# Performance work log

Measured on AMD Instinct MI355X. Metric: run time of the kernel, lower is better.

## Reference

```python
import jax, jax.numpy as jnp
import numpy as np

N, M, K = 4096, 256, 32
W_EPS = 1e-6


def _spd(key, n, k):
    # well-conditioned SPD precision matrices: A A^T / k + I
    a = jax.random.normal(key, (n, k, k), dtype=jnp.float32)
    return jnp.matmul(a, jnp.swapaxes(a, -1, -2)) / k + jnp.eye(k, dtype=jnp.float32)


def setup_inputs() -> dict:
    key = jax.random.key(0)
    k1, k2, k3, k4 = jax.random.split(key, 4)
    W = jax.random.uniform(k1, (N, M), dtype=jnp.float32)
    mu_s = jax.random.normal(k2, (N, K), dtype=jnp.float32)
    omega_child = _spd(k3, N, K)
    omega_parent = _spd(k4, M, K)
    return {"W": W, "mu_s": mu_s, "omega_child": omega_child, "omega_parent": omega_parent}


def reference(W, mu_s, omega_child, omega_parent):
    # mask out negligible memberships (original skips w < 1e-6)
    wT = W.T                                   # (M, N)
    mask = wT >= W_EPS
    w = jnp.where(mask, wT, 0.0)

    # v_i = inv(omega_child_i) @ mu_s_i  -> batched solve, (N, K)
    v = jnp.linalg.solve(omega_child, mu_s[..., None])[..., 0]

    # transported means: Omega_alpha @ v_i, (M, N, K)
    T = jnp.einsum('mkl,nl->mnk', omega_parent, v)

    Z = w.sum(-1)                              # (M,)
    Zs = jnp.maximum(Z, 1e-30)
    mu_bar = jnp.einsum('mn,mnk->mk', w, T) / Zs[:, None]
    diff = T - mu_bar[:, None, :]              # (M, N, K)
    var = jnp.einsum('mn,mnk->mk', w, diff * diff) / Zs[:, None]
    psi = var.sum(-1)                          # (M,)

    # clusters with fewer than 2 contributing agents get psi = 0
    count = mask.sum(-1)
    return jnp.where(count >= 2, psi, 0.0)
```

## Files before the change

kernel.cpp:

```cpp
#include <hip/hip_runtime.h>

constexpr int N_AG = 4096;
constexpr int M_CL = 256;
constexpr int KD   = 32;
constexpr float WEPS = 1e-6f;

constexpr int PART_STRIDE = 1088;
constexpr int VT_OFF = M_CL * 4 * PART_STRIDE;
constexpr int WT_OFF = VT_OFF + N_AG * KD;

typedef __attribute__((ext_vector_type(8))) short short8;
typedef __attribute__((ext_vector_type(4))) float f32x4;

__device__ __forceinline__ float rlane(float x, int l) {
    return __int_as_float(__builtin_amdgcn_readlane(__float_as_int(x), l));
}
__device__ __forceinline__ short8 mk8(unsigned a, unsigned b, unsigned c, unsigned d) {
    union { unsigned u[4]; short8 s; } x;
    x.u[0] = a; x.u[1] = b; x.u[2] = c; x.u[3] = d;
    return x.s;
}

template<int J>
struct GJ2 {
    static __device__ __forceinline__ void run(float (&ca)[32], float (&cb)[32]) {
        const float pa = rlane(ca[J], J);
        const float pb = rlane(cb[J], J);
        const float ia = 1.0f / pa;
        const float ib = 1.0f / pb;
        ca[J] *= ia;
        cb[J] *= ib;
        #pragma unroll
        for (int i = 0; i < 32; ++i) {
            if (i == J) continue;
            const float fa = rlane(ca[i], J);
            const float fb = rlane(cb[i], J);
            ca[i] = fmaf(-fa, ca[J], ca[i]);
            cb[i] = fmaf(-fb, cb[J], cb[i]);
        }
        GJ2<J + 1>::run(ca, cb);
    }
};
template<> struct GJ2<32> {
    static __device__ __forceinline__ void run(float (&)[32], float (&)[32]) {}
};

__global__ __launch_bounds__(256, 1) void solve_transpose_kernel(
        const float* __restrict__ oc, const float* __restrict__ mu,
        const float* __restrict__ W,
        float* __restrict__ vT, float* __restrict__ Wt) {
    __shared__ float res8[32][8];
    __shared__ float tb[32][33];

    const int t    = threadIdx.x;
    const int lane = t & 63;
    const int wv   = t >> 6;
    const int idx0 = blockIdx.x * 8;
    const int ia_  = idx0 + 2 * wv;
    const int ib_  = ia_ + 1;
    const int c = (lane < 32) ? lane : 32;

    float ca[32], cb[32];
    #pragma unroll
    for (int i = 0; i < 32; ++i) {
        ca[i] = (c < 32) ? oc[ia_ * 1024 + i * 32 + c] : mu[ia_ * 32 + i];
        cb[i] = (c < 32) ? oc[ib_ * 1024 + i * 32 + c] : mu[ib_ * 32 + i];
    }

    GJ2<0>::run(ca, cb);

    float ra = 0.0f, rb = 0.0f;
    #pragma unroll
    for (int i = 0; i < 32; ++i) {
        const float xa = rlane(ca[i], 32);
        const float xb = rlane(cb[i], 32);
        if (lane == i) { ra = xa; rb = xb; }
    }
    if (lane < 32) {
        res8[lane][2 * wv]     = ra;
        res8[lane][2 * wv + 1] = rb;
    }
    __syncthreads();
    {
        const int k = t >> 3, j = t & 7;
        vT[(size_t)k * 4096 + idx0 + j] = res8[k][j];
    }

    const int x = t & 31, y = t >> 5;
    #pragma unroll
    for (int rep = 0; rep < 2; ++rep) {
        const int tile = blockIdx.x * 2 + rep;
        const int n0 = (tile & 127) * 32;
        const int m0 = (tile >> 7) * 32;
        __syncthreads();
        #pragma unroll
        for (int r = 0; r < 4; ++r) {
            const int n = y + 8 * r;
            const float w = W[(size_t)(n0 + n) * 256 + m0 + x];
            tb[n][x] = (w >= WEPS) ? w : 0.0f;
        }
        __syncthreads();
        #pragma unroll
        for (int r = 0; r < 4; ++r) {
            const int mm = y + 8 * r;
            Wt[(size_t)(m0 + mm) * 4096 + n0 + x] = tb[x][mm];
        }
    }
}

__global__ __launch_bounds__(256, 4) void partial_kernel(const float* __restrict__ Wt,
                                                         const float* __restrict__ vT,
                                                         float* __restrict__ wsout) {
    const int m = blockIdx.x >> 2;
    const int p = blockIdx.x & 3;
    const int t = threadIdx.x;
    const int lane = t & 63;
    const int wv   = t >> 6;

    __shared__ float swbuf[1024];
    __shared__ float sred[4 * 1024];
    __shared__ float red[256];
    __shared__ float s1buf[32];

    const float4 wv4 = reinterpret_cast<const float4*>(Wt + (size_t)m * 4096 + p * 1024)[t];
    const float zacc = wv4.x + wv4.y + wv4.z + wv4.w;
    const float cacc = (wv4.x >= WEPS ? 1.f : 0.f) + (wv4.y >= WEPS ? 1.f : 0.f)
                     + (wv4.z >= WEPS ? 1.f : 0.f) + (wv4.w >= WEPS ? 1.f : 0.f);
    reinterpret_cast<float4*>(swbuf)[t] =
        make_float4(sqrtf(wv4.x), sqrtf(wv4.y), sqrtf(wv4.z), sqrtf(wv4.w));
    if (t < 32) s1buf[t] = 0.0f;
    __syncthreads();

    const int a = lane & 15;
    const int g = lane >> 4;
    const int nl = wv * 256 + g * 8;

    const float4* pa4 = reinterpret_cast<const float4*>(vT + (size_t)a * 4096 + p * 1024 + nl);
    const float4* pb4 = reinterpret_cast<const float4*>(vT + (size_t)(a + 16) * 4096 + p * 1024 + nl);

    f32x4 Chh[4], Chl[4];
    #pragma unroll
    for (int q = 0; q < 4; ++q) {
        Chh[q] = (f32x4){0.f, 0.f, 0.f, 0.f};
        Chl[q] = (f32x4){0.f, 0.f, 0.f, 0.f};
    }
    float s1a = 0.0f, s1b = 0.0f;

    #pragma unroll 2
    for (int ch = 0; ch < 8; ++ch) {
        const float4 va0 = pa4[ch * 8];
        const float4 va1 = pa4[ch * 8 + 1];
        const float4 vb0 = pb4[ch * 8];
        const float4 vb1 = pb4[ch * 8 + 1];
        const float4 s0  = *reinterpret_cast<const float4*>(&swbuf[nl + ch * 32]);
        const float4 s1v = *reinterpret_cast<const float4*>(&swbuf[nl + ch * 32 + 4]);

        const float ua0 = va0.x * s0.x,  ua1 = va0.y * s0.y;
        const float ua2 = va0.z * s0.z,  ua3 = va0.w * s0.w;
        const float ua4 = va1.x * s1v.x, ua5 = va1.y * s1v.y;
        const float ua6 = va1.z * s1v.z, ua7 = va1.w * s1v.w;
        const float ub0 = vb0.x * s0.x,  ub1 = vb0.y * s0.y;
        const float ub2 = vb0.z * s0.z,  ub3 = vb0.w * s0.w;
        const float ub4 = vb1.x * s1v.x, ub5 = vb1.y * s1v.y;
        const float ub6 = vb1.z * s1v.z, ub7 = vb1.w * s1v.w;

        s1a += s0.x*ua0 + s0.y*ua1 + s0.z*ua2 + s0.w*ua3
             + s1v.x*ua4 + s1v.y*ua5 + s1v.z*ua6 + s1v.w*ua7;
        s1b += s0.x*ub0 + s0.y*ub1 + s0.z*ub2 + s0.w*ub3
             + s1v.x*ub4 + s1v.y*ub5 + s1v.z*ub6 + s1v.w*ub7;

        #define BITS(u) __float_as_uint(u)
        #define LO(u)  ((u) - __uint_as_float(BITS(u) & 0xFFFF0000u))
        const short8 h0 = mk8(
            __builtin_amdgcn_perm(BITS(ua1), BITS(ua0), 0x07060302u),
            __builtin_amdgcn_perm(BITS(ua3), BITS(ua2), 0x07060302u),
            __builtin_amdgcn_perm(BITS(ua5), BITS(ua4), 0x07060302u),
            __builtin_amdgcn_perm(BITS(ua7), BITS(ua6), 0x07060302u));
        const short8 h1 = mk8(
            __builtin_amdgcn_perm(BITS(ub1), BITS(ub0), 0x07060302u),
            __builtin_amdgcn_perm(BITS(ub3), BITS(ub2), 0x07060302u),
            __builtin_amdgcn_perm(BITS(ub5), BITS(ub4), 0x07060302u),
            __builtin_amdgcn_perm(BITS(ub7), BITS(ub6), 0x07060302u));
        const float la0 = LO(ua0), la1 = LO(ua1), la2 = LO(ua2), la3 = LO(ua3);
        const float la4 = LO(ua4), la5 = LO(ua5), la6 = LO(ua6), la7 = LO(ua7);
        const float lb0 = LO(ub0), lb1 = LO(ub1), lb2 = LO(ub2), lb3 = LO(ub3);
        const float lb4 = LO(ub4), lb5 = LO(ub5), lb6 = LO(ub6), lb7 = LO(ub7);
        const short8 l0 = mk8(
            __builtin_amdgcn_perm(BITS(la1), BITS(la0), 0x07060302u),
            __builtin_amdgcn_perm(BITS(la3), BITS(la2), 0x07060302u),
            __builtin_amdgcn_perm(BITS(la5), BITS(la4), 0x07060302u),
            __builtin_amdgcn_perm(BITS(la7), BITS(la6), 0x07060302u));
        const short8 l1 = mk8(
            __builtin_amdgcn_perm(BITS(lb1), BITS(lb0), 0x07060302u),
            __builtin_amdgcn_perm(BITS(lb3), BITS(lb2), 0x07060302u),
            __builtin_amdgcn_perm(BITS(lb5), BITS(lb4), 0x07060302u),
            __builtin_amdgcn_perm(BITS(lb7), BITS(lb6), 0x07060302u));
        #undef BITS
        #undef LO

        Chh[0] = __builtin_amdgcn_mfma_f32_16x16x32_bf16(h0, h0, Chh[0], 0, 0, 0);
        Chh[1] = __builtin_amdgcn_mfma_f32_16x16x32_bf16(h0, h1, Chh[1], 0, 0, 0);
        Chh[2] = __builtin_amdgcn_mfma_f32_16x16x32_bf16(h1, h0, Chh[2], 0, 0, 0);
        Chh[3] = __builtin_amdgcn_mfma_f32_16x16x32_bf16(h1, h1, Chh[3], 0, 0, 0);
        Chl[0] = __builtin_amdgcn_mfma_f32_16x16x32_bf16(h0, l0, Chl[0], 0, 0, 0);
        Chl[1] = __builtin_amdgcn_mfma_f32_16x16x32_bf16(h0, l1, Chl[1], 0, 0, 0);
        Chl[2] = __builtin_amdgcn_mfma_f32_16x16x32_bf16(h1, l0, Chl[2], 0, 0, 0);
        Chl[3] = __builtin_amdgcn_mfma_f32_16x16x32_bf16(h1, l1, Chl[3], 0, 0, 0);
    }

    s1a += __shfl_xor(s1a, 16); s1a += __shfl_xor(s1a, 32);
    s1b += __shfl_xor(s1b, 16); s1b += __shfl_xor(s1b, 32);
    if (lane < 16) {
        atomicAdd(&s1buf[a], s1a);
        atomicAdd(&s1buf[a + 16], s1b);
    }

    float* rw = &sred[wv * 1024];
    #pragma unroll
    for (int q = 0; q < 4; ++q) {
        const int I = q >> 1, J = q & 1;
        #pragma unroll
        for (int r = 0; r < 4; ++r) {
            const int ar = I * 16 + (lane >> 4) * 4 + r;
            const int br = J * 16 + (lane & 15);
            rw[ar * 32 + br] = Chh[q][r] + Chl[q][r];
        }
    }
    __syncthreads();
    #pragma unroll
    for (int q = 0; q < 4; ++q) {
        const int I = q >> 1, J = q & 1;
        #pragma unroll
        for (int r = 0; r < 4; ++r) {
            const int ar = I * 16 + (lane >> 4) * 4 + r;
            const int br = J * 16 + (lane & 15);
            rw[br * 32 + ar] += Chl[q][r];
        }
    }
    __syncthreads();

    const size_t base = (size_t)(m * 4 + p) * PART_STRIDE;
    float o0 = 0.f, o1 = 0.f, o2 = 0.f, o3 = 0.f;
    #pragma unroll
    for (int ww = 0; ww < 4; ++ww) {
        const float4 x = *reinterpret_cast<const float4*>(&sred[ww * 1024 + t * 4]);
        o0 += x.x; o1 += x.y; o2 += x.z; o3 += x.w;
    }
    *reinterpret_cast<float4*>(&wsout[base + t * 4]) = make_float4(o0, o1, o2, o3);

    red[t] = zacc; __syncthreads();
    #pragma unroll
    for (int s = 128; s > 0; s >>= 1) {
        if (t < s) red[t] += red[t + s];
        __syncthreads();
    }
    if (t == 0) wsout[base + 1056] = red[0];
    __syncthreads();
    red[t] = cacc; __syncthreads();
    #pragma unroll
    for (int s = 128; s > 0; s >>= 1) {
        if (t < s) red[t] += red[t + s];
        __syncthreads();
    }
    if (t == 0) wsout[base + 1057] = red[0];
    if (t < 32) wsout[base + 1024 + t] = s1buf[t];
}

__global__ __launch_bounds__(256) void combine_kernel(const float* __restrict__ op,
                                                      const float* __restrict__ ws,
                                                      float* __restrict__ out) {
    const int m = blockIdx.x;
    const int t = threadIdx.x;

    __shared__ float omg[32 * 33];
    __shared__ float vbar[32];
    __shared__ float red[256];

    #pragma unroll
    for (int i = 0; i < 4; ++i) {
        const int g = t + 256 * i;
        const int r = g >> 5, cc = g & 31;
        omg[r * 33 + cc] = op[(size_t)m * 1024 + g];
    }

    const size_t mb = (size_t)m * 4 * PART_STRIDE;
    float Z = 0.0f, cnt = 0.0f, s1 = 0.0f;
    float s2[4] = {0.f, 0.f, 0.f, 0.f};
    #pragma unroll
    for (int p2 = 0; p2 < 4; ++p2) {
        const size_t bp = mb + (size_t)p2 * PART_STRIDE;
        Z   += ws[bp + 1056];
        cnt += ws[bp + 1057];
        if (t < 32) s1 += ws[bp + 1024 + t];
        const float4 sp = *reinterpret_cast<const float4*>(&ws[bp + t * 4]);
        s2[0] += sp.x; s2[1] += sp.y; s2[2] += sp.z; s2[3] += sp.w;
    }
    const float invZ = 1.0f / fmaxf(Z, 1e-30f);
    if (t < 32) vbar[t] = s1 * invZ;
    __syncthreads();

    const int k  = t >> 3;
    const int l0 = (t & 7) * 4;
    float G[4] = {0.f, 0.f, 0.f, 0.f};
    #pragma unroll
    for (int i = 0; i < 32; ++i) {
        const float ok = omg[i * 33 + k];
        #pragma unroll
        for (int q = 0; q < 4; ++q) G[q] = fmaf(ok, omg[i * 33 + l0 + q], G[q]);
    }

    const float vk = vbar[k];
    float val = 0.0f;
    #pragma unroll
    for (int q = 0; q < 4; ++q)
        val += G[q] * (s2[q] * invZ - vk * vbar[l0 + q]);

    red[t] = val; __syncthreads();
    #pragma unroll
    for (int s = 128; s > 0; s >>= 1) {
        if (t < s) red[t] += red[t + s];
        __syncthreads();
    }
    if (t == 0) out[m] = (cnt >= 1.5f) ? red[0] : 0.0f;
}

extern "C" void kernel_launch(void* const* d_in, const int* in_sizes, int n_in,
                              void* d_out, int out_size, void* d_ws, size_t ws_size,
                              hipStream_t stream) {
    const float* W  = (const float*)d_in[0];
    const float* mu = (const float*)d_in[1];
    const float* oc = (const float*)d_in[2];
    const float* op = (const float*)d_in[3];
    float* out = (float*)d_out;
    float* ws  = (float*)d_ws;

    solve_transpose_kernel<<<512, 256, 0, stream>>>(oc, mu, W, ws + VT_OFF, ws + WT_OFF);
    partial_kernel<<<1024, 256, 0, stream>>>(ws + WT_OFF, ws + VT_OFF, ws);
    combine_kernel<<<256, 256, 0, stream>>>(op, ws, out);
}
```

Before: 115.6 us.

## Fuse three kernels into one cooperative launch with grid syncs

Merges the solve/transpose, partial-moment and combine kernels into a single cooperative kernel of 512 blocks that separates the phases with grid-wide barriers. Shared memory is a union of the three phase layouts. To fit the grid, the partial phase now gives each block half of a cluster's agents instead of a quarter, so it uses 512 blocks instead of 1024 and the combine step reads two partials per cluster. The goal is to remove launch gaps between kernels, at the cost of grid-sync overhead and less parallelism in the middle phase, with a three-kernel fallback if the cooperative launch fails.

```diff
diff --git a/kernel.cpp b/kernel.cpp
--- a/kernel.cpp
+++ b/kernel.cpp
@@ -1,4 +1,6 @@
 #include <hip/hip_runtime.h>
+#include <hip/hip_cooperative_groups.h>
+namespace cg = cooperative_groups;
 
 constexpr int N_AG = 4096;
 constexpr int M_CL = 256;
@@ -6,7 +8,7 @@
 constexpr float WEPS = 1e-6f;
 
 constexpr int PART_STRIDE = 1088;
-constexpr int VT_OFF = M_CL * 4 * PART_STRIDE;
+constexpr int VT_OFF = M_CL * 2 * PART_STRIDE;
 constexpr int WT_OFF = VT_OFF + N_AG * KD;
 
 typedef __attribute__((ext_vector_type(8))) short short8;
@@ -20,6 +22,11 @@
     x.u[0] = a; x.u[1] = b; x.u[2] = c; x.u[3] = d;
     return x.s;
 }
+
+struct SmemA { float res8[32][8]; float tb[32][33]; };
+struct SmemB { float swbuf[2048]; float sred[4096]; float red[256]; float s1buf[32]; };
+struct SmemC { float omg[32 * 33]; float vbar[32]; float red[256]; };
+union SmemU { SmemA a; SmemB b; SmemC c; };
 
 template<int J>
 struct GJ2 {
@@ -45,17 +52,13 @@
     static __device__ __forceinline__ void run(float (&)[32], float (&)[32]) {}
 };
 
-__global__ __launch_bounds__(256, 1) void solve_transpose_kernel(
+__device__ __forceinline__ void phaseA(int bid, int t,
         const float* __restrict__ oc, const float* __restrict__ mu,
         const float* __restrict__ W,
-        float* __restrict__ vT, float* __restrict__ Wt) {
-    __shared__ float res8[32][8];
-    __shared__ float tb[32][33];
-
-    const int t    = threadIdx.x;
+        float* __restrict__ vT, float* __restrict__ Wt, SmemA& s) {
     const int lane = t & 63;
     const int wv   = t >> 6;
-    const int idx0 = blockIdx.x * 8;
+    const int idx0 = bid * 8;
     const int ia_  = idx0 + 2 * wv;
     const int ib_  = ia_ + 1;
     const int c = (lane < 32) ? lane : 32;
@@ -77,19 +80,19 @@
         if (lane == i) { ra = xa; rb = xb; }
     }
     if (lane < 32) {
-        res8[lane][2 * wv]     = ra;
-        res8[lane][2 * wv + 1] = rb;
+        s.res8[lane][2 * wv]     = ra;
+        s.res8[lane][2 * wv + 1] = rb;
     }
     __syncthreads();
     {
         const int k = t >> 3, j = t & 7;
-        vT[(size_t)k * 4096 + idx0 + j] = res8[k][j];
+        vT[(size_t)k * 4096 + idx0 + j] = s.res8[k][j];
     }
 
     const int x = t & 31, y = t >> 5;
     #pragma unroll
     for (int rep = 0; rep < 2; ++rep) {
-        const int tile = blockIdx.x * 2 + rep;
+        const int tile = bid * 2 + rep;
         const int n0 = (tile & 127) * 32;
         const int m0 = (tile >> 7) * 32;
         __syncthreads();
@@ -97,46 +100,45 @@
         for (int r = 0; r < 4; ++r) {
             const int n = y + 8 * r;
             const float w = W[(size_t)(n0 + n) * 256 + m0 + x];
-            tb[n][x] = (w >= WEPS) ? w : 0.0f;
+            s.tb[n][x] = (w >= WEPS) ? w : 0.0f;
         }
         __syncthreads();
         #pragma unroll
         for (int r = 0; r < 4; ++r) {
             const int mm = y + 8 * r;
-            Wt[(size_t)(m0 + mm) * 4096 + n0 + x] = tb[x][mm];
-        }
-    }
-}
-
-__global__ __launch_bounds__(256, 4) void partial_kernel(const float* __restrict__ Wt,
-                                                         const float* __restrict__ vT,
-                                                         float* __restrict__ wsout) {
-    const int m = blockIdx.x >> 2;
-    const int p = blockIdx.x & 3;
-    const int t = threadIdx.x;
+            Wt[(size_t)(m0 + mm) * 4096 + n0 + x] = s.tb[x][mm];
+        }
+    }
+}
+
+__device__ __forceinline__ void phaseB(int task, int t,
+        const float* __restrict__ Wt, const float* __restrict__ vT,
+        float* __restrict__ wsout, SmemB& s) {
+    const int m = task >> 1;
+    const int h = task & 1;
     const int lane = t & 63;
     const int wv   = t >> 6;
 
-    __shared__ float swbuf[1024];
-    __shared__ float sred[4 * 1024];
-    __shared__ float red[256];
-    __shared__ float s1buf[32];
-
-    const float4 wv4 = reinterpret_cast<const float4*>(Wt + (size_t)m * 4096 + p * 1024)[t];
-    const float zacc = wv4.x + wv4.y + wv4.z + wv4.w;
-    const float cacc = (wv4.x >= WEPS ? 1.f : 0.f) + (wv4.y >= WEPS ? 1.f : 0.f)
-                     + (wv4.z >= WEPS ? 1.f : 0.f) + (wv4.w >= WEPS ? 1.f : 0.f);
-    reinterpret_cast<float4*>(swbuf)[t] =
-        make_float4(sqrtf(wv4.x), sqrtf(wv4.y), sqrtf(wv4.z), sqrtf(wv4.w));
-    if (t < 32) s1buf[t] = 0.0f;
+    const float* wrow = Wt + (size_t)m * 4096 + h * 2048;
+    float zacc = 0.0f, cacc = 0.0f;
+    #pragma unroll
+    for (int i = 0; i < 2; ++i) {
+        const float4 w4 = reinterpret_cast<const float4*>(wrow)[t + 256 * i];
+        zacc += w4.x + w4.y + w4.z + w4.w;
+        cacc += (w4.x >= WEPS ? 1.f : 0.f) + (w4.y >= WEPS ? 1.f : 0.f)
+              + (w4.z >= WEPS ? 1.f : 0.f) + (w4.w >= WEPS ? 1.f : 0.f);
+        reinterpret_cast<float4*>(s.swbuf)[t + 256 * i] =
+            make_float4(sqrtf(w4.x), sqrtf(w4.y), sqrtf(w4.z), sqrtf(w4.w));
+    }
+    if (t < 32) s.s1buf[t] = 0.0f;
     __syncthreads();
 
     const int a = lane & 15;
     const int g = lane >> 4;
-    const int nl = wv * 256 + g * 8;
-
-    const float4* pa4 = reinterpret_cast<const float4*>(vT + (size_t)a * 4096 + p * 1024 + nl);
-    const float4* pb4 = reinterpret_cast<const float4*>(vT + (size_t)(a + 16) * 4096 + p * 1024 + nl);
+    const int nl = wv * 512 + g * 8;
+
+    const float4* pa4 = reinterpret_cast<const float4*>(vT + (size_t)a * 4096 + h * 2048 + nl);
+    const float4* pb4 = reinterpret_cast<const float4*>(vT + (size_t)(a + 16) * 4096 + h * 2048 + nl);
 
     f32x4 Chh[4], Chl[4];
     #pragma unroll
@@ -147,13 +149,13 @@
     float s1a = 0.0f, s1b = 0.0f;
 
     #pragma unroll 2
-    for (int ch = 0; ch < 8; ++ch) {
+    for (int ch = 0; ch < 16; ++ch) {
         const float4 va0 = pa4[ch * 8];
         const float4 va1 = pa4[ch * 8 + 1];
         const float4 vb0 = pb4[ch * 8];
         const float4 vb1 = pb4[ch * 8 + 1];
-        const float4 s0  = *reinterpret_cast<const float4*>(&swbuf[nl + ch * 32]);
-        const float4 s1v = *reinterpret_cast<const float4*>(&swbuf[nl + ch * 32 + 4]);
+        const float4 s0  = *reinterpret_cast<const float4*>(&s.swbuf[nl + ch * 32]);
+        const float4 s1v = *reinterpret_cast<const float4*>(&s.swbuf[nl + ch * 32 + 4]);
 
         const float ua0 = va0.x * s0.x,  ua1 = va0.y * s0.y;
         const float ua2 = va0.z * s0.z,  ua3 = va0.w * s0.w;
@@ -211,11 +213,11 @@
     s1a += __shfl_xor(s1a, 16); s1a += __shfl_xor(s1a, 32);
     s1b += __shfl_xor(s1b, 16); s1b += __shfl_xor(s1b, 32);
     if (lane < 16) {
-        atomicAdd(&s1buf[a], s1a);
-        atomicAdd(&s1buf[a + 16], s1b);
-    }
-
-    float* rw = &sred[wv * 1024];
+        atomicAdd(&s.s1buf[a], s1a);
+        atomicAdd(&s.s1buf[a + 16], s1b);
+    }
+
+    float* rw = &s.sred[wv * 1024];
     #pragma unroll
     for (int q = 0; q < 4; ++q) {
         const int I = q >> 1, J = q & 1;
@@ -239,55 +241,48 @@
     }
     __syncthreads();
 
-    const size_t base = (size_t)(m * 4 + p) * PART_STRIDE;
+    const size_t base = (size_t)task * PART_STRIDE;
     float o0 = 0.f, o1 = 0.f, o2 = 0.f, o3 = 0.f;
     #pragma unroll
     for (int ww = 0; ww < 4; ++ww) {
-        const float4 x = *reinterpret_cast<const float4*>(&sred[ww * 1024 + t * 4]);
+        const float4 x = *reinterpret_cast<const float4*>(&s.sred[ww * 1024 + t * 4]);
         o0 += x.x; o1 += x.y; o2 += x.z; o3 += x.w;
     }
     *reinterpret_cast<float4*>(&wsout[base + t * 4]) = make_float4(o0, o1, o2, o3);
 
-    red[t] = zacc; __syncthreads();
-    #pragma unroll
-    for (int s = 128; s > 0; s >>= 1) {
-        if (t < s) red[t] += red[t + s];
-        __syncthreads();
-    }
-    if (t == 0) wsout[base + 1056] = red[0];
-    __syncthreads();
-    red[t] = cacc; __syncthreads();
-    #pragma unroll
-    for (int s = 128; s > 0; s >>= 1) {
-        if (t < s) red[t] += red[t + s];
-        __syncthreads();
-    }
-    if (t == 0) wsout[base + 1057] = red[0];
-    if (t < 32) wsout[base + 1024 + t] = s1buf[t];
-}
-
-__global__ __launch_bounds__(256) void combine_kernel(const float* __restrict__ op,
-                                                      const float* __restrict__ ws,
-                                                      float* __restrict__ out) {
-    const int m = blockIdx.x;
-    const int t = threadIdx.x;
-
-    __shared__ float omg[32 * 33];
-    __shared__ float vbar[32];
-    __shared__ float red[256];
-
+    s.red[t] = zacc; __syncthreads();
+    #pragma unroll
+    for (int st = 128; st > 0; st >>= 1) {
+        if (t < st) s.red[t] += s.red[t + st];
+        __syncthreads();
+    }
+    if (t == 0) wsout[base + 1056] = s.red[0];
+    __syncthreads();
+    s.red[t] = cacc; __syncthreads();
+    #pragma unroll
+    for (int st = 128; st > 0; st >>= 1) {
+        if (t < st) s.red[t] += s.red[t + st];
+        __syncthreads();
+    }
+    if (t == 0) wsout[base + 1057] = s.red[0];
+    if (t < 32) wsout[base + 1024 + t] = s.s1buf[t];
+}
+
+__device__ __forceinline__ void phaseC(int m, int t,
+        const float* __restrict__ op, const float* __restrict__ ws,
+        float* __restrict__ out, SmemC& s) {
     #pragma unroll
     for (int i = 0; i < 4; ++i) {
-        const int g = t + 256 * i;
-        const int r = g >> 5, cc = g & 31;
-        omg[r * 33 + cc] = op[(size_t)m * 1024 + g];
-    }
-
-    const size_t mb = (size_t)m * 4 * PART_STRIDE;
+        const int gg = t + 256 * i;
+        const int r = gg >> 5, cc = gg & 31;
+        s.omg[r * 33 + cc] = op[(size_t)m * 1024 + gg];
+    }
+
+    const size_t mb = (size_t)m * 2 * PART_STRIDE;
     float Z = 0.0f, cnt = 0.0f, s1 = 0.0f;
     float s2[4] = {0.f, 0.f, 0.f, 0.f};
     #pragma unroll
-    for (int p2 = 0; p2 < 4; ++p2) {
+    for (int p2 = 0; p2 < 2; ++p2) {
         const size_t bp = mb + (size_t)p2 * PART_STRIDE;
         Z   += ws[bp + 1056];
         cnt += ws[bp + 1057];
@@ -296,7 +291,7 @@
         s2[0] += sp.x; s2[1] += sp.y; s2[2] += sp.z; s2[3] += sp.w;
     }
     const float invZ = 1.0f / fmaxf(Z, 1e-30f);
-    if (t < 32) vbar[t] = s1 * invZ;
+    if (t < 32) s.vbar[t] = s1 * invZ;
     __syncthreads();
 
     const int k  = t >> 3;
@@ -304,24 +299,61 @@
     float G[4] = {0.f, 0.f, 0.f, 0.f};
     #pragma unroll
     for (int i = 0; i < 32; ++i) {
-        const float ok = omg[i * 33 + k];
-        #pragma unroll
-        for (int q = 0; q < 4; ++q) G[q] = fmaf(ok, omg[i * 33 + l0 + q], G[q]);
-    }
-
-    const float vk = vbar[k];
+        const float ok = s.omg[i * 33 + k];
+        #pragma unroll
+        for (int q = 0; q < 4; ++q) G[q] = fmaf(ok, s.omg[i * 33 + l0 + q], G[q]);
+    }
+
+    const float vk = s.vbar[k];
     float val = 0.0f;
     #pragma unroll
     for (int q = 0; q < 4; ++q)
-        val += G[q] * (s2[q] * invZ - vk * vbar[l0 + q]);
-
-    red[t] = val; __syncthreads();
-    #pragma unroll
-    for (int s = 128; s > 0; s >>= 1) {
-        if (t < s) red[t] += red[t + s];
-        __syncthreads();
-    }
-    if (t == 0) out[m] = (cnt >= 1.5f) ? red[0] : 0.0f;
+        val += G[q] * (s2[q] * invZ - vk * s.vbar[l0 + q]);
+
+    s.red[t] = val; __syncthreads();
+    #pragma unroll
+    for (int st = 128; st > 0; st >>= 1) {
+        if (t < st) s.red[t] += s.red[t + st];
+        __syncthreads();
+    }
+    if (t == 0) out[m] = (cnt >= 1.5f) ? s.red[0] : 0.0f;
+}
+
+__global__ __launch_bounds__(256, 2) void fused_kernel(
+        const float* __restrict__ W, const float* __restrict__ mu,
+        const float* __restrict__ oc, const float* __restrict__ op,
+        float* __restrict__ out, float* __restrict__ ws) {
+    __shared__ SmemU smem;
+    cg::grid_group grid = cg::this_grid();
+    const int bid = blockIdx.x;
+    const int t = threadIdx.x;
+    float* vT = ws + VT_OFF;
+    float* Wt = ws + WT_OFF;
+
+    phaseA(bid, t, oc, mu, W, vT, Wt, smem.a);
+    __threadfence();
+    grid.sync();
+    phaseB(bid, t, Wt, vT, ws, smem.b);
+    __threadfence();
+    grid.sync();
+    if (bid < 256) phaseC(bid, t, op, ws, out, smem.c);
+}
+
+__global__ __launch_bounds__(256, 2) void kA(const float* __restrict__ oc,
+        const float* __restrict__ mu, const float* __restrict__ W,
+        float* __restrict__ vT, float* __restrict__ Wt) {
+    __shared__ SmemA s;
+    phaseA(blockIdx.x, threadIdx.x, oc, mu, W, vT, Wt, s);
+}
+__global__ __launch_bounds__(256, 2) void kB(const float* __restrict__ Wt,
+        const float* __restrict__ vT, float* __restrict__ ws) {
+    __shared__ SmemB s;
+    phaseB(blockIdx.x, threadIdx.x, Wt, vT, ws, s);
+}
+__global__ __launch_bounds__(256) void kC(const float* __restrict__ op,
+        const float* __restrict__ ws, float* __restrict__ out) {
+    __shared__ SmemC s;
+    phaseC(blockIdx.x, threadIdx.x, op, ws, out, s);
 }
 
 extern "C" void kernel_launch(void* const* d_in, const int* in_sizes, int n_in,
@@ -334,7 +366,14 @@
     float* out = (float*)d_out;
     float* ws  = (float*)d_ws;
 
-    solve_transpose_kernel<<<512, 256, 0, stream>>>(oc, mu, W, ws + VT_OFF, ws + WT_OFF);
-    partial_kernel<<<1024, 256, 0, stream>>>(ws + WT_OFF, ws + VT_OFF, ws);
-    combine_kernel<<<256, 256, 0, stream>>>(op, ws, out);
-}
+    void* kargs[] = { (void*)&W, (void*)&mu, (void*)&oc, (void*)&op,
+                      (void*)&out, (void*)&ws };
+    hipError_t e = hipLaunchCooperativeKernel(
+        reinterpret_cast<void*>(fused_kernel), dim3(512), dim3(256),
+        kargs, 0, stream);
+    if (e != hipSuccess) {
+        kA<<<512, 256, 0, stream>>>(oc, mu, W, ws + VT_OFF, ws + WT_OFF);
+        kB<<<512, 256, 0, stream>>>(ws + WT_OFF, ws + VT_OFF, ws);
+        kC<<<256, 256, 0, stream>>>(op, ws, out);
+    }
+}
```

Measured after the change: 294.1 us. +154.4%, slower.
